# Kernel optimization log

Hardware: AMD Instinct MI355X
Metric: run time of the kernel (lower is better)

Reference implementation:

```python
import jax, jax.numpy as jnp
import numpy as np

N, E, G = 20000, 100000, 32
HID, HEADS, HC = 64, 8, 64  # hidden, heads, per-head channels (PyG: out_channels per head)
L, K = 3, 4


def setup_inputs() -> dict:
    key = jax.random.key(0)
    ks = jax.random.split(key, 20)
    rn = lambda k, s, sc=0.05: jax.random.normal(k, s, jnp.float32) * sc
    HO = HEADS * HC  # 512
    return {
        "x": jax.random.uniform(ks[0], (N, 7), jnp.float32),
        "edge_attr": jax.random.normal(ks[1], (E, 4), jnp.float32),
        "means": jax.random.normal(ks[2], (K, 8), jnp.float32),
        "log_stds": jnp.zeros((K, 8), jnp.float32),
        "sp_W": rn(ks[3], (K, HID), 0.3), "sp_b": jnp.zeros((HID,), jnp.float32),
        "ne_W": rn(ks[4], (7, HID), 0.3), "ne_b": jnp.zeros((HID,), jnp.float32),
        "ee_W": rn(ks[5], (4, HID), 0.3), "ee_b": jnp.zeros((HID,), jnp.float32),
        "Wq": rn(ks[6], (L, HID, HO)), "bq": jnp.zeros((L, HO), jnp.float32),
        "Wk": rn(ks[7], (L, HID, HO)), "bk": jnp.zeros((L, HO), jnp.float32),
        "Wv": rn(ks[8], (L, HID, HO)), "bv": jnp.zeros((L, HO), jnp.float32),
        "We": rn(ks[9], (L, HID, HO)), "be": jnp.zeros((L, HO), jnp.float32),
        "Ws": rn(ks[10], (L, HID, HID)), "bs": jnp.zeros((L, HID), jnp.float32),
        "eu_W": rn(ks[11], (L, 3 * HID, HID)), "eu_b": jnp.zeros((L, HID), jnp.float32),
        "rW1": rn(ks[12], (2 * HID, HID)), "rb1": jnp.zeros((HID,), jnp.float32),
        "rW2": rn(ks[13], (HID, HID)), "rb2": jnp.zeros((HID,), jnp.float32),
        "rW3": rn(ks[14], (HID, 2)), "rb3": jnp.zeros((2,), jnp.float32),
        "edge_index": jax.random.randint(ks[15], (2, E), 0, N, jnp.int32),
        "batch": jnp.sort(jax.random.randint(ks[16], (N,), 0, G, jnp.int32)),
        "num_graphs": G,
    }


def reference(x, edge_attr, means, log_stds, sp_W, sp_b, ne_W, ne_b, ee_W, ee_b,
              Wq, bq, Wk, bk, Wv, bv, We, be, Ws, bs, eu_W, eu_b,
              rW1, rb1, rW2, rb2, rW3, rb3, edge_index, batch, num_graphs):
    n = x.shape[0]
    src, dst = edge_index[0], edge_index[1]

    # ---- SpatialGaussianEncoder (dropout is identity in eval) ----
    p = x[:, :4]
    sl, sr = p[src, :2], p[src, 2:4]
    dl, dr = p[dst, :2], p[dst, 2:4]
    rel = jnp.stack([dl - sl, dl - sr, dr - sl, dr - sr], axis=1)  # [E,4,2]
    dist = jnp.linalg.norm(rel, axis=-1)                           # [E,4]
    ang = jnp.arctan2(rel[..., 1], rel[..., 0])                    # [E,4]
    u = jnp.stack([dist, ang], axis=-1).reshape(-1, 8)             # [E,8] (d,a)x4
    std = jnp.exp(log_stds) + 1e-6                                 # [K,8]
    z = (u[:, None, :] - means[None]) / std[None]                  # [E,K,8]
    w = jnp.exp(-0.5 * jnp.sum(z * z, axis=-1))                    # [E,K]
    sp = jax.nn.relu(w @ sp_W + sp_b)                              # [E,HID]

    h = jax.nn.relu(x @ ne_W + ne_b)                               # [N,HID]
    ea = jax.nn.relu(edge_attr @ ee_W + ee_b) + sp                 # [E,HID]

    scale = 1.0 / float(np.sqrt(HC))
    for l in range(L):
        # PyG TransformerConv(hidden, hidden, heads=8, edge_dim=hidden, concat=False)
        q = (h @ Wq[l] + bq[l]).reshape(n, HEADS, HC)
        k = (h @ Wk[l] + bk[l]).reshape(n, HEADS, HC)
        v = (h @ Wv[l] + bv[l]).reshape(n, HEADS, HC)
        e = (ea @ We[l] + be[l]).reshape(-1, HEADS, HC)
        kj = k[src] + e                                            # [E,H,C]
        alpha = jnp.einsum('ehc,ehc->eh', q[dst], kj) * scale      # [E,H]
        m = jax.ops.segment_max(alpha, dst, num_segments=n)
        ex = jnp.exp(alpha - m[dst])
        den = jax.ops.segment_sum(ex, dst, num_segments=n)
        a = ex / (den[dst] + 1e-16)                                # scatter-softmax over dst
        msg = a[:, :, None] * (v[src] + e)                         # [E,H,C]
        out = jax.ops.segment_sum(msg, dst, num_segments=n).mean(axis=1)  # concat=False -> head mean
        h = jax.nn.relu(out + h @ Ws[l] + bs[l])                   # skip (root_weight) + F.relu
        ef = jnp.concatenate([h[src], h[dst], ea], axis=1)         # [E,3*HID]
        ea = jax.nn.relu(ef @ eu_W[l] + eu_b[l])

    # ---- per-graph masked-mean pooling == segment mean ----
    cn = jnp.maximum(jax.ops.segment_sum(jnp.ones((n,), x.dtype), batch, num_segments=num_graphs), 1.0)
    node_pool = jax.ops.segment_sum(h, batch, num_segments=num_graphs) / cn[:, None]
    eb = batch[src]
    ce = jnp.maximum(jax.ops.segment_sum(jnp.ones((src.shape[0],), x.dtype), eb, num_segments=num_graphs), 1.0)
    edge_pool = jax.ops.segment_sum(ea, eb, num_segments=num_graphs) / ce[:, None]
    g = jnp.concatenate([node_pool, edge_pool], axis=1)            # [G,2*HID]

    h1 = jax.nn.relu(g @ rW1 + rb1)
    h2 = jax.nn.relu(h1 @ rW2 + rb2)
    return jnp.tanh(h2 @ rW3 + rb3)                                # [G,2]
```

## Files before the change

kernel.cpp:

```cpp
#include <hip/hip_runtime.h>
#include <hip/hip_bf16.h>
#include <cstdint>
#include <cstddef>



__global__ void __launch_bounds__(256) k_node_embed(
    const float* __restrict__ x, const float* __restrict__ neW, const float* __restrict__ neb,
    float* __restrict__ h, int N)
{
    int idx = blockIdx.x * 256 + threadIdx.x;
    int n = idx >> 6, c = idx & 63;
    if (n >= N) return;
    float acc = neb[c];
    #pragma unroll
    for (int j = 0; j < 7; ++j) acc += x[(size_t)n * 7 + j] * neW[j * 64 + c];
    h[(size_t)n * 64 + c] = fmaxf(acc, 0.f);
}

__global__ void __launch_bounds__(256) k_edge_w(
    const float* __restrict__ x,
    const float* __restrict__ means, const float* __restrict__ log_stds,
    const int* __restrict__ src, const int* __restrict__ dst,
    float* __restrict__ wbuf, int E)
{
    int e = blockIdx.x * 256 + threadIdx.x;
    if (e >= E) return;
    int s = src[e], d = dst[e];
    const float* ps = x + (size_t)s * 7;
    const float* pd = x + (size_t)d * 7;
    float slx = ps[0], sly = ps[1], srx = ps[2], sry = ps[3];
    float dlx = pd[0], dly = pd[1], drx = pd[2], dry = pd[3];
    float u[8];
    float rx, ry;
    rx = dlx - slx; ry = dly - sly; u[0] = sqrtf(rx*rx + ry*ry); u[1] = atan2f(ry, rx);
    rx = dlx - srx; ry = dly - sry; u[2] = sqrtf(rx*rx + ry*ry); u[3] = atan2f(ry, rx);
    rx = drx - slx; ry = dry - sly; u[4] = sqrtf(rx*rx + ry*ry); u[5] = atan2f(ry, rx);
    rx = drx - srx; ry = dry - sry; u[6] = sqrtf(rx*rx + ry*ry); u[7] = atan2f(ry, rx);
    #pragma unroll
    for (int kk = 0; kk < 4; ++kk) {
        float ssum = 0.f;
        #pragma unroll
        for (int dd = 0; dd < 8; ++dd) {
            float stdv = expf(log_stds[kk*8+dd]) + 1e-6f;
            float z = (u[dd] - means[kk*8+dd]) / stdv;
            ssum += z * z;
        }
        wbuf[(size_t)e*4 + kk] = expf(-0.5f * ssum);
    }
}

__global__ void __launch_bounds__(256) k_edge_ea(
    const float* __restrict__ edge_attr, const float* __restrict__ wbuf,
    const float* __restrict__ spW, const float* __restrict__ spb,
    const float* __restrict__ eeW, const float* __restrict__ eeb,
    float* __restrict__ ea, int E)
{
    int idx = blockIdx.x * 256 + threadIdx.x;
    int e = idx >> 6, c = idx & 63;
    if (e >= E) return;
    float acce = eeb[c];
    #pragma unroll
    for (int j = 0; j < 4; ++j) acce += edge_attr[(size_t)e*4 + j] * eeW[j*64 + c];
    float accs = spb[c];
    #pragma unroll
    for (int j = 0; j < 4; ++j) accs += wbuf[(size_t)e*4 + j] * spW[j*64 + c];
    ea[(size_t)e*64 + c] = fmaxf(acce, 0.f) + fmaxf(accs, 0.f);
}


__global__ void __launch_bounds__(256) k_hist(
    const int* __restrict__ dst, int* __restrict__ deg, int E)
{
    int e = blockIdx.x * 256 + threadIdx.x;
    if (e < E) atomicAdd(deg + dst[e], 1);
}

__global__ void __launch_bounds__(1024) k_scan(
    const int* __restrict__ deg, int* __restrict__ ptr, int* __restrict__ headw, int N)
{
    __shared__ int part[1024];
    int t = threadIdx.x;
    int per = (N + 1023) / 1024;
    int s = 0;
    for (int i = 0; i < per; ++i) { int idx = t*per + i; if (idx < N) s += deg[idx]; }
    part[t] = s;
    __syncthreads();
    for (int off = 1; off < 1024; off <<= 1) {
        int v = (t >= off) ? part[t - off] : 0;
        __syncthreads();
        part[t] += v;
        __syncthreads();
    }
    int base = (t > 0) ? part[t - 1] : 0;
    for (int i = 0; i < per; ++i) {
        int idx = t*per + i;
        if (idx < N) { ptr[idx] = base; headw[idx] = base; base += deg[idx]; }
    }
    if (t == 1023) ptr[N] = part[1023];
}

__global__ void __launch_bounds__(256) k_scatter(
    const int* __restrict__ dst, const int* __restrict__ src, const int* __restrict__ batch,
    int* __restrict__ headw, int* __restrict__ perm, int* __restrict__ srcg,
    int* __restrict__ ieb, int E)
{
    int e = blockIdx.x * 256 + threadIdx.x;
    if (e < E) {
        int s = src[e];
        int pos = atomicAdd(headw + dst[e], 1);
        perm[pos] = e;
        srcg[pos] = s;
        ieb[e] = batch[s];
    }
}


__global__ void __launch_bounds__(256) k_wprod_all(
    const float* __restrict__ Wq, const float* __restrict__ bq,
    const float* __restrict__ Wk, const float* __restrict__ We,
    float* __restrict__ Mk, float* __restrict__ Me,
    float* __restrict__ bqk, float* __restrict__ bqe)
{
    int h = blockIdx.x;
    int which = blockIdx.y;
    int l = blockIdx.z;
    const float* Wq_l = Wq + (size_t)l * 64 * 512;
    const float* bq_l = bq + (size_t)l * 512;
    const float* Wx_l = (which ? We : Wk) + (size_t)l * 64 * 512;
    float* M  = (which ? Me : Mk) + (size_t)l * 64 * 512;
    float* bM = (which ? bqe : bqk) + (size_t)l * 512;
    __shared__ float wq_s[65][64];
    __shared__ float wx_s[64][65];
    int tid = threadIdx.x;
    for (int i = tid; i < 4096; i += 256) {
        int r = i >> 6, c2 = i & 63;
        wq_s[r][c2] = Wq_l[(size_t)r*512 + h*64 + c2];
        wx_s[r][c2] = Wx_l[(size_t)r*512 + h*64 + c2];
    }
    if (tid < 64) wq_s[64][tid] = bq_l[h*64 + tid];
    __syncthreads();
    int j = tid & 63, cg = tid >> 6;
    for (int c = cg*16; c < cg*16 + 16; ++c) {
        float s = 0.f;
        #pragma unroll 8
        for (int c2 = 0; c2 < 64; ++c2) s += wq_s[c][c2] * wx_s[j][c2];
        M[(size_t)c*512 + h*64 + j] = s;
    }
    if (tid < 64) {
        float s = 0.f;
        #pragma unroll 8
        for (int c2 = 0; c2 < 64; ++c2) s += wq_s[64][c2] * wx_s[tid][c2];
        bM[h*64 + tid] = s;
    }
}

__global__ void __launch_bounds__(64) k_wqb_all(
    const float* __restrict__ Wq, const float* __restrict__ bq,
    const float* __restrict__ bk, const float* __restrict__ be,
    float* __restrict__ wqb, float* __restrict__ cb)
{
    int l = blockIdx.x;
    const float* Wq_l = Wq + (size_t)l * 64 * 512;
    const float* bq_l = bq + (size_t)l * 512;
    const float* bk_l = bk + (size_t)l * 512;
    const float* be_l = be + (size_t)l * 512;
    float* wqb_l = wqb + (size_t)l * 512;
    float* cb_l  = cb + (size_t)l * 8;
    int c = threadIdx.x;
    for (int h = 0; h < 8; ++h) {
        float s = 0.f;
        for (int c2 = 0; c2 < 64; ++c2)
            s += Wq_l[(size_t)c*512 + h*64 + c2] * (bk_l[h*64+c2] + be_l[h*64+c2]);
        wqb_l[c*8 + h] = s;
    }
    if (c < 8) {
        float s = 0.f;
        for (int c2 = 0; c2 < 64; ++c2)
            s += bq_l[c*64 + c2] * (bk_l[c*64+c2] + be_l[c*64+c2]);
        cb_l[c] = s;
    }
}

__global__ void __launch_bounds__(256) k_qb(
    const float* __restrict__ h, const float* __restrict__ wqb, const float* __restrict__ cb,
    float* __restrict__ qbv, int N)
{
    int idx = blockIdx.x * 256 + threadIdx.x;
    int n = idx >> 3, hh = idx & 7;
    if (n >= N) return;
    float s = cb[hh];
    #pragma unroll 8
    for (int c = 0; c < 64; ++c) s += h[(size_t)n*64 + c] * wqb[c*8 + hh];
    qbv[(size_t)n*8 + hh] = s;
}


__global__ void __launch_bounds__(256) k_gemm512_dual(
    const float* __restrict__ X,
    const float* __restrict__ W0, const float* __restrict__ b0p, float* __restrict__ Y0,
    const float* __restrict__ W1, const float* __restrict__ b1p, float* __restrict__ Y1,
    int M)
{
    const float* W    = blockIdx.y ? W1 : W0;
    const float* bias = blockIdx.y ? b1p : b0p;
    float* Y          = blockIdx.y ? Y1 : Y0;
    __shared__ __align__(16) float xs[32][64];
    int tid = threadIdx.x;
    int r0 = blockIdx.x * 32;
    for (int i = tid; i < 2048; i += 256) {
        int r = i >> 6, c = i & 63;
        int rr = r0 + r;
        xs[r][c] = (rr < M) ? X[(size_t)rr * 64 + c] : 0.f;
    }
    __syncthreads();
    int wv = tid >> 6, lane = tid & 63;
    int c0 = lane * 8;
    float acc[8][8];
    float4 b0 = *(const float4*)(bias + c0);
    float4 b1 = *(const float4*)(bias + c0 + 4);
    #pragma unroll
    for (int t = 0; t < 8; ++t) {
        acc[t][0]=b0.x; acc[t][1]=b0.y; acc[t][2]=b0.z; acc[t][3]=b0.w;
        acc[t][4]=b1.x; acc[t][5]=b1.y; acc[t][6]=b1.z; acc[t][7]=b1.w;
    }
    #pragma unroll 2
    for (int j = 0; j < 64; ++j) {
        float4 wa = *(const float4*)(W + (size_t)j*512 + c0);
        float4 wb = *(const float4*)(W + (size_t)j*512 + c0 + 4);
        #pragma unroll
        for (int t = 0; t < 8; ++t) {
            float a = xs[wv*8 + t][j];
            acc[t][0] += a*wa.x; acc[t][1] += a*wa.y; acc[t][2] += a*wa.z; acc[t][3] += a*wa.w;
            acc[t][4] += a*wb.x; acc[t][5] += a*wb.y; acc[t][6] += a*wb.z; acc[t][7] += a*wb.w;
        }
    }
    #pragma unroll
    for (int t = 0; t < 8; ++t) {
        int r = r0 + wv*8 + t;
        if (r < M) {
            float4 o0 = {acc[t][0],acc[t][1],acc[t][2],acc[t][3]};
            float4 o1 = {acc[t][4],acc[t][5],acc[t][6],acc[t][7]};
            *(float4*)(Y + (size_t)r*512 + c0)     = o0;
            *(float4*)(Y + (size_t)r*512 + c0 + 4) = o1;
        }
    }
}


__global__ void __launch_bounds__(256) k_attn_fused(
    const float* __restrict__ qk, const float* __restrict__ qe2, const float* __restrict__ qbv,
    const float* __restrict__ ea, const float* __restrict__ hbuf,
    const int* __restrict__ ptr, const int* __restrict__ perm, const int* __restrict__ srcg,
    float* __restrict__ hagg, float* __restrict__ tbuf, float* __restrict__ sbuf, int N)
{
    int wv = threadIdx.x >> 6, lane = threadIdx.x & 63;
    int n = blockIdx.x * 4 + wv;
    if (n >= N) return;
    int h = lane >> 3, p = lane & 7;
    int b = ptr[n], e_ = ptr[n + 1];
    const float4* xp = (const float4*)(qk + (size_t)n*512 + lane*8);
    float4 x0 = xp[0], x1 = xp[1];
    const float4* gp = (const float4*)(qe2 + (size_t)n*512 + lane*8);
    float4 g0 = gp[0], g1 = gp[1];
    float qbh = qbv[(size_t)n*8 + h];
    float m = -3.4e38f, den = 0.f;
    float hacc[8], tacc[8];
    #pragma unroll
    for (int i = 0; i < 8; ++i) { hacc[i] = 0.f; tacc[i] = 0.f; }
    for (int it = b; it < e_; ++it) {
        int s = srcg[it];
        int e = perm[it];
        const float4* hp = (const float4*)(hbuf + (size_t)s*64 + p*8);
        float4 h0 = hp[0], h1 = hp[1];
        const float4* ap = (const float4*)(ea + (size_t)e*64 + p*8);
        float4 a0 = ap[0], a1 = ap[1];
        float t = x0.x*h0.x + x0.y*h0.y + x0.z*h0.z + x0.w*h0.w
                + x1.x*h1.x + x1.y*h1.y + x1.z*h1.z + x1.w*h1.w
                + g0.x*a0.x + g0.y*a0.y + g0.z*a0.z + g0.w*a0.w
                + g1.x*a1.x + g1.y*a1.y + g1.z*a1.z + g1.w*a1.w;
        t += __shfl_xor(t, 1);
        t += __shfl_xor(t, 2);
        t += __shfl_xor(t, 4);
        float al = 0.125f * (t + qbh);
        float mn = fmaxf(m, al);
        float r = expf(m - mn);
        float w = expf(al - mn);
        den = den * r + w;
        m = mn;
        hacc[0] = hacc[0]*r + w*h0.x; hacc[1] = hacc[1]*r + w*h0.y;
        hacc[2] = hacc[2]*r + w*h0.z; hacc[3] = hacc[3]*r + w*h0.w;
        hacc[4] = hacc[4]*r + w*h1.x; hacc[5] = hacc[5]*r + w*h1.y;
        hacc[6] = hacc[6]*r + w*h1.z; hacc[7] = hacc[7]*r + w*h1.w;
        tacc[0] = tacc[0]*r + w*a0.x; tacc[1] = tacc[1]*r + w*a0.y;
        tacc[2] = tacc[2]*r + w*a0.z; tacc[3] = tacc[3]*r + w*a0.w;
        tacc[4] = tacc[4]*r + w*a1.x; tacc[5] = tacc[5]*r + w*a1.y;
        tacc[6] = tacc[6]*r + w*a1.z; tacc[7] = tacc[7]*r + w*a1.w;
    }
    float inv = 0.125f / (den + 1e-16f);
    float4 o;
    o = {hacc[0]*inv,hacc[1]*inv,hacc[2]*inv,hacc[3]*inv};
    *(float4*)(hagg + (size_t)n*512 + lane*8)     = o;
    o = {hacc[4]*inv,hacc[5]*inv,hacc[6]*inv,hacc[7]*inv};
    *(float4*)(hagg + (size_t)n*512 + lane*8 + 4) = o;
    o = {tacc[0]*inv,tacc[1]*inv,tacc[2]*inv,tacc[3]*inv};
    *(float4*)(tbuf + (size_t)n*512 + lane*8)     = o;
    o = {tacc[4]*inv,tacc[5]*inv,tacc[6]*inv,tacc[7]*inv};
    *(float4*)(tbuf + (size_t)n*512 + lane*8 + 4) = o;
    if (p == 0) sbuf[(size_t)n*8 + h] = den * inv;
}

__global__ void __launch_bounds__(256) k_nf_gemm2(
    const float* __restrict__ tbuf, const float* __restrict__ hagg,
    const float* __restrict__ We, const float* __restrict__ Wv,
    float* __restrict__ pbuf, int N)
{
    __shared__ float As[64][132];
    __shared__ __align__(16) float Wt[64][64];
    int tid = threadIdx.x;
    int g = blockIdx.y;
    int n0 = blockIdx.x * 128;
    int wv = tid >> 6, lane = tid & 63;
    int rg = lane >> 3, cg = lane & 7;
    int c0 = cg * 8;
    int rbase = wv * 32 + rg * 4;
    float acc[4][8];
    #pragma unroll
    for (int t = 0; t < 4; ++t)
        #pragma unroll
        for (int i = 0; i < 8; ++i) acc[t][i] = 0.f;
    #pragma unroll
    for (int yy = 0; yy < 2; ++yy) {
        int y = g * 2 + yy;
        #pragma unroll
        for (int round = 0; round < 2; ++round) {
            const float* A = round ? hagg : tbuf;
            const float* W = round ? Wv : We;
            {
                int rt = tid & 127;
                int n = n0 + rt;
                int jh = (tid >> 7) * 32;
                if (n < N) {
                    const float* ap = A + (size_t)n*512 + y*64;
                    #pragma unroll
                    for (int j4 = 0; j4 < 8; ++j4) {
                        int j = jh + j4 * 4;
                        float4 a = *(const float4*)(ap + j);
                        As[j+0][rt] = a.x; As[j+1][rt] = a.y;
                        As[j+2][rt] = a.z; As[j+3][rt] = a.w;
                    }
                } else {
                    #pragma unroll
                    for (int j4 = 0; j4 < 8; ++j4) {
                        int j = jh + j4 * 4;
                        As[j+0][rt] = 0.f; As[j+1][rt] = 0.f;
                        As[j+2][rt] = 0.f; As[j+3][rt] = 0.f;
                    }
                }
                #pragma unroll
                for (int i = 0; i < 4; ++i) {
                    int idx = tid + i * 256;
                    int j = idx >> 4, c4 = (idx & 15) * 4;
                    *(float4*)&Wt[j][c4] = *(const float4*)(W + (size_t)j*512 + y*64 + c4);
                }
            }
            __syncthreads();
            #pragma unroll 4
            for (int j = 0; j < 64; ++j) {
                float4 av = *(const float4*)&As[j][rbase];
                float4 w0 = *(const float4*)&Wt[j][c0];
                float4 w1 = *(const float4*)&Wt[j][c0 + 4];
                acc[0][0] += av.x*w0.x; acc[0][1] += av.x*w0.y; acc[0][2] += av.x*w0.z; acc[0][3] += av.x*w0.w;
                acc[0][4] += av.x*w1.x; acc[0][5] += av.x*w1.y; acc[0][6] += av.x*w1.z; acc[0][7] += av.x*w1.w;
                acc[1][0] += av.y*w0.x; acc[1][1] += av.y*w0.y; acc[1][2] += av.y*w0.z; acc[1][3] += av.y*w0.w;
                acc[1][4] += av.y*w1.x; acc[1][5] += av.y*w1.y; acc[1][6] += av.y*w1.z; acc[1][7] += av.y*w1.w;
                acc[2][0] += av.z*w0.x; acc[2][1] += av.z*w0.y; acc[2][2] += av.z*w0.z; acc[2][3] += av.z*w0.w;
                acc[2][4] += av.z*w1.x; acc[2][5] += av.z*w1.y; acc[2][6] += av.z*w1.z; acc[2][7] += av.z*w1.w;
                acc[3][0] += av.w*w0.x; acc[3][1] += av.w*w0.y; acc[3][2] += av.w*w0.z; acc[3][3] += av.w*w0.w;
                acc[3][4] += av.w*w1.x; acc[3][5] += av.w*w1.y; acc[3][6] += av.w*w1.z; acc[3][7] += av.w*w1.w;
            }
            __syncthreads();
        }
    }
    float* out = pbuf + (size_t)g * N * 64;
    #pragma unroll
    for (int t = 0; t < 4; ++t) {
        int n = n0 + rbase + t;
        if (n < N) {
            float4 o0 = {acc[t][0],acc[t][1],acc[t][2],acc[t][3]};
            float4 o1 = {acc[t][4],acc[t][5],acc[t][6],acc[t][7]};
            *(float4*)(out + (size_t)n*64 + c0)     = o0;
            *(float4*)(out + (size_t)n*64 + c0 + 4) = o1;
        }
    }
}

__global__ void __launch_bounds__(256) k_nf_reduce2(
    const float* __restrict__ pbuf, const float* __restrict__ hin,
    const float* __restrict__ sbuf, const float* __restrict__ Ws,
    const float* __restrict__ be, const float* __restrict__ bv,
    const float* __restrict__ bs, float* __restrict__ hnext, int N)
{
    int idx = blockIdx.x * 256 + threadIdx.x;
    int n = idx >> 6, cc = idx & 63;
    if (n >= N) return;
    float a = bs[cc];
    #pragma unroll
    for (int y = 0; y < 4; ++y) a += pbuf[(size_t)y*N*64 + (size_t)n*64 + cc];
    float hv = hin[(size_t)n*64 + cc];
    #pragma unroll 8
    for (int j = 0; j < 64; ++j) a += __shfl(hv, j) * Ws[(size_t)j*64 + cc];
    #pragma unroll
    for (int h = 0; h < 8; ++h)
        a += sbuf[(size_t)n*8 + h] * (be[h*64 + cc] + bv[h*64 + cc]);
    hnext[(size_t)n*64 + cc] = fmaxf(a, 0.f);
}

__global__ void __launch_bounds__(256) k_eu_pre(
    const float* __restrict__ h, const float* __restrict__ euW,
    float* __restrict__ hw, int N)
{
    __shared__ float As[64][132];
    __shared__ __align__(16) float Wt[64][64];
    int tid = threadIdx.x;
    int y = blockIdx.y;
    int n0 = blockIdx.x * 128;
    {
        int rt = tid & 127;
        int n = n0 + rt;
        int jh = (tid >> 7) * 32;
        if (n < N) {
            const float* ap = h + (size_t)n*64;
            #pragma unroll
            for (int j4 = 0; j4 < 8; ++j4) {
                int j = jh + j4 * 4;
                float4 a = *(const float4*)(ap + j);
                As[j+0][rt] = a.x; As[j+1][rt] = a.y;
                As[j+2][rt] = a.z; As[j+3][rt] = a.w;
            }
        } else {
            #pragma unroll
            for (int j4 = 0; j4 < 8; ++j4) {
                int j = jh + j4 * 4;
                As[j+0][rt] = 0.f; As[j+1][rt] = 0.f;
                As[j+2][rt] = 0.f; As[j+3][rt] = 0.f;
            }
        }
        #pragma unroll
        for (int i = 0; i < 4; ++i) {
            int idx = tid + i * 256;
            *(float4*)&Wt[idx >> 4][(idx & 15) * 4] =
                *(const float4*)(euW + (size_t)y*4096 + idx * 4);
        }
    }
    __syncthreads();
    int wv = tid >> 6, lane = tid & 63;
    int rg = lane >> 3, cg = lane & 7;
    int c0 = cg * 8;
    int rbase = wv * 32 + rg * 4;
    float acc[4][8];
    #pragma unroll
    for (int t = 0; t < 4; ++t)
        #pragma unroll
        for (int i = 0; i < 8; ++i) acc[t][i] = 0.f;
    #pragma unroll 4
    for (int j = 0; j < 64; ++j) {
        float4 av = *(const float4*)&As[j][rbase];
        float4 w0 = *(const float4*)&Wt[j][c0];
        float4 w1 = *(const float4*)&Wt[j][c0 + 4];
        acc[0][0] += av.x*w0.x; acc[0][1] += av.x*w0.y; acc[0][2] += av.x*w0.z; acc[0][3] += av.x*w0.w;
        acc[0][4] += av.x*w1.x; acc[0][5] += av.x*w1.y; acc[0][6] += av.x*w1.z; acc[0][7] += av.x*w1.w;
        acc[1][0] += av.y*w0.x; acc[1][1] += av.y*w0.y; acc[1][2] += av.y*w0.z; acc[1][3] += av.y*w0.w;
        acc[1][4] += av.y*w1.x; acc[1][5] += av.y*w1.y; acc[1][6] += av.y*w1.z; acc[1][7] += av.y*w1.w;
        acc[2][0] += av.z*w0.x; acc[2][1] += av.z*w0.y; acc[2][2] += av.z*w0.z; acc[2][3] += av.z*w0.w;
        acc[2][4] += av.z*w1.x; acc[2][5] += av.z*w1.y; acc[2][6] += av.z*w1.z; acc[2][7] += av.z*w1.w;
        acc[3][0] += av.w*w0.x; acc[3][1] += av.w*w0.y; acc[3][2] += av.w*w0.z; acc[3][3] += av.w*w0.w;
        acc[3][4] += av.w*w1.x; acc[3][5] += av.w*w1.y; acc[3][6] += av.w*w1.z; acc[3][7] += av.w*w1.w;
    }
    #pragma unroll
    for (int t = 0; t < 4; ++t) {
        int n = n0 + rbase + t;
        if (n < N) {
            float4 o0 = {acc[t][0],acc[t][1],acc[t][2],acc[t][3]};
            float4 o1 = {acc[t][4],acc[t][5],acc[t][6],acc[t][7]};
            *(float4*)(hw + (size_t)n*128 + y*64 + c0)     = o0;
            *(float4*)(hw + (size_t)n*128 + y*64 + c0 + 4) = o1;
        }
    }
}

__global__ void __launch_bounds__(256) k_edge_update2(
    const float* __restrict__ hw, const float* __restrict__ ea,
    const float* __restrict__ euW2, const float* __restrict__ eub,
    const int* __restrict__ src, const int* __restrict__ dst,
    float* __restrict__ ea2, int E)
{
    __shared__ float As[64][132];
    __shared__ __align__(16) float Wt[64][64];
    __shared__ int sid[128], did[128];
    int tid = threadIdx.x;
    int e0 = blockIdx.x * 128;
    if (tid < 128) {
        int e = e0 + tid; if (e >= E) e = E - 1;
        sid[tid] = src[e]; did[tid] = dst[e];
    }
    {
        int et = tid & 127;
        int e = e0 + et; if (e >= E) e = E - 1;
        const float* ap = ea + (size_t)e * 64;
        int jh = (tid >> 7) * 32;
        #pragma unroll
        for (int j4 = 0; j4 < 8; ++j4) {
            int j = jh + j4 * 4;
            float4 a = *(const float4*)(ap + j);
            As[j+0][et] = a.x; As[j+1][et] = a.y;
            As[j+2][et] = a.z; As[j+3][et] = a.w;
        }
        #pragma unroll
        for (int i = 0; i < 4; ++i) {
            int idx = tid + i * 256;
            *(float4*)&Wt[idx >> 4][(idx & 15) * 4] = *(const float4*)(euW2 + idx * 4);
        }
    }
    __syncthreads();
    int wv = tid >> 6, lane = tid & 63;
    int rg = lane >> 3, cg = lane & 7;
    int c0 = cg * 8;
    int rbase = wv * 32 + rg * 4;
    float acc[4][8];
    float4 b0 = *(const float4*)(eub + c0);
    float4 b1 = *(const float4*)(eub + c0 + 4);
    #pragma unroll
    for (int t = 0; t < 4; ++t) {
        acc[t][0]=b0.x; acc[t][1]=b0.y; acc[t][2]=b0.z; acc[t][3]=b0.w;
        acc[t][4]=b1.x; acc[t][5]=b1.y; acc[t][6]=b1.z; acc[t][7]=b1.w;
    }
    #pragma unroll 4
    for (int j = 0; j < 64; ++j) {
        float4 av = *(const float4*)&As[j][rbase];
        float4 w0 = *(const float4*)&Wt[j][c0];
        float4 w1 = *(const float4*)&Wt[j][c0 + 4];
        acc[0][0] += av.x*w0.x; acc[0][1] += av.x*w0.y; acc[0][2] += av.x*w0.z; acc[0][3] += av.x*w0.w;
        acc[0][4] += av.x*w1.x; acc[0][5] += av.x*w1.y; acc[0][6] += av.x*w1.z; acc[0][7] += av.x*w1.w;
        acc[1][0] += av.y*w0.x; acc[1][1] += av.y*w0.y; acc[1][2] += av.y*w0.z; acc[1][3] += av.y*w0.w;
        acc[1][4] += av.y*w1.x; acc[1][5] += av.y*w1.y; acc[1][6] += av.y*w1.z; acc[1][7] += av.y*w1.w;
        acc[2][0] += av.z*w0.x; acc[2][1] += av.z*w0.y; acc[2][2] += av.z*w0.z; acc[2][3] += av.z*w0.w;
        acc[2][4] += av.z*w1.x; acc[2][5] += av.z*w1.y; acc[2][6] += av.z*w1.z; acc[2][7] += av.z*w1.w;
        acc[3][0] += av.w*w0.x; acc[3][1] += av.w*w0.y; acc[3][2] += av.w*w0.z; acc[3][3] += av.w*w0.w;
        acc[3][4] += av.w*w1.x; acc[3][5] += av.w*w1.y; acc[3][6] += av.w*w1.z; acc[3][7] += av.w*w1.w;
    }
    #pragma unroll
    for (int t = 0; t < 4; ++t) {
        int e = e0 + rbase + t;
        if (e < E) {
            int s = sid[rbase + t], d = did[rbase + t];
            const float4* sp = (const float4*)(hw + (size_t)s*128 + c0);
            const float4* dp = (const float4*)(hw + (size_t)d*128 + 64 + c0);
            float4 s0 = sp[0], s1 = sp[1];
            float4 d0 = dp[0], d1 = dp[1];
            float4 o0 = {fmaxf(acc[t][0]+s0.x+d0.x,0.f), fmaxf(acc[t][1]+s0.y+d0.y,0.f),
                         fmaxf(acc[t][2]+s0.z+d0.z,0.f), fmaxf(acc[t][3]+s0.w+d0.w,0.f)};
            float4 o1 = {fmaxf(acc[t][4]+s1.x+d1.x,0.f), fmaxf(acc[t][5]+s1.y+d1.y,0.f),
                         fmaxf(acc[t][6]+s1.z+d1.z,0.f), fmaxf(acc[t][7]+s1.w+d1.w,0.f)};
            *(float4*)(ea2 + (size_t)e*64 + c0)     = o0;
            *(float4*)(ea2 + (size_t)e*64 + c0 + 4) = o1;
        }
    }
}


__global__ void __launch_bounds__(64) k_node_pool(
    const float* __restrict__ h, const int* __restrict__ batch,
    float* __restrict__ npool, float* __restrict__ cn, int N)
{
    int lane = threadIdx.x;
    int n0 = blockIdx.x * 64;
    float acc = 0.f; int cur = -1; int run = 0;
    for (int i = 0; i < 64; ++i) {
        int n = n0 + i;
        if (n >= N) break;
        int b = batch[n];
        if (b != cur) {
            if (cur >= 0) {
                atomicAdd(npool + (size_t)cur*64 + lane, acc);
                if (lane == 0) atomicAdd(cn + cur, (float)run);
            }
            cur = b; acc = 0.f; run = 0;
        }
        acc += h[(size_t)n*64 + lane];
        ++run;
    }
    if (cur >= 0) {
        atomicAdd(npool + (size_t)cur*64 + lane, acc);
        if (lane == 0) atomicAdd(cn + cur, (float)run);
    }
}

__global__ void __launch_bounds__(256) k_edge_pool2(
    const float* __restrict__ ea, const int* __restrict__ ieb,
    float* __restrict__ rep, int E)
{
    __shared__ float pool_s[32][64];
    __shared__ float cnt_s[32];
    int tid = threadIdx.x;
    for (int i = tid; i < 2048; i += 256) ((float*)pool_s)[i] = 0.f;
    if (tid < 32) cnt_s[tid] = 0.f;
    __syncthreads();
    int wv = tid >> 6, lane = tid & 63;
    int base = blockIdx.x * 64 + wv * 16;
    int b16[16]; float v16[16];
    #pragma unroll
    for (int u = 0; u < 16; ++u) {
        int e = base + u;
        bool ok = (e < E);
        b16[u] = ok ? ieb[e] : -1;
        v16[u] = ok ? ea[(size_t)e*64 + lane] : 0.f;
    }
    #pragma unroll
    for (int u = 0; u < 16; ++u) {
        if (b16[u] >= 0) {
            atomicAdd(&pool_s[b16[u]][lane], v16[u]);
            if (lane == 0) atomicAdd(&cnt_s[b16[u]], 1.f);
        }
    }
    __syncthreads();
    float* myrep = rep + (size_t)(blockIdx.x & 7) * 2080;
    for (int i = tid; i < 2048; i += 256) atomicAdd(myrep + i, ((float*)pool_s)[i]);
    if (tid < 32) atomicAdd(myrep + 2048 + tid, cnt_s[tid]);
}

__global__ void __launch_bounds__(256) k_pool_merge(
    const float* __restrict__ rep, float* __restrict__ epool, float* __restrict__ ce)
{
    int i = blockIdx.x * 256 + threadIdx.x;
    if (i < 2080) {
        float s = 0.f;
        #pragma unroll
        for (int r = 0; r < 8; ++r) s += rep[(size_t)r*2080 + i];
        if (i < 2048) epool[i] = s; else ce[i - 2048] = s;
    }
}

__global__ void __launch_bounds__(64) k_head_mlp(
    const float* __restrict__ npool, const float* __restrict__ epool,
    const float* __restrict__ cn, const float* __restrict__ ce,
    const float* __restrict__ rW1, const float* __restrict__ rb1,
    const float* __restrict__ rW2, const float* __restrict__ rb2,
    const float* __restrict__ rW3, const float* __restrict__ rb3,
    float* __restrict__ out)
{
    __shared__ float g[128];
    __shared__ float h1[64];
    __shared__ float h2[64];
    int b = blockIdx.x, lane = threadIdx.x;
    float cnv = fmaxf(cn[b], 1.f), cev = fmaxf(ce[b], 1.f);
    g[lane]      = npool[(size_t)b*64 + lane] / cnv;
    g[64 + lane] = epool[(size_t)b*64 + lane] / cev;
    __syncthreads();
    float acc = rb1[lane];
    #pragma unroll 4
    for (int j = 0; j < 128; ++j) acc += g[j] * rW1[j*64 + lane];
    h1[lane] = fmaxf(acc, 0.f);
    __syncthreads();
    acc = rb2[lane];
    #pragma unroll 4
    for (int j = 0; j < 64; ++j) acc += h1[j] * rW2[j*64 + lane];
    h2[lane] = fmaxf(acc, 0.f);
    __syncthreads();
    if (lane < 2) {
        float o = rb3[lane];
        for (int j = 0; j < 64; ++j) o += h2[j] * rW3[j*2 + lane];
        out[b*2 + lane] = tanhf(o);
    }
}


extern "C" void kernel_launch(void* const* d_in, const int* in_sizes, int n_in,
                              void* d_out, int out_size, void* d_ws, size_t ws_size,
                              hipStream_t stream)
{
    const float* x         = (const float*)d_in[0];
    const float* edge_attr = (const float*)d_in[1];
    const float* means     = (const float*)d_in[2];
    const float* log_stds  = (const float*)d_in[3];
    const float* spW       = (const float*)d_in[4];
    const float* spb       = (const float*)d_in[5];
    const float* neW       = (const float*)d_in[6];
    const float* neb       = (const float*)d_in[7];
    const float* eeW       = (const float*)d_in[8];
    const float* eeb       = (const float*)d_in[9];
    const float* Wq        = (const float*)d_in[10];
    const float* bq        = (const float*)d_in[11];
    const float* Wk        = (const float*)d_in[12];
    const float* bk        = (const float*)d_in[13];
    const float* Wv        = (const float*)d_in[14];
    const float* bv        = (const float*)d_in[15];
    const float* We        = (const float*)d_in[16];
    const float* be        = (const float*)d_in[17];
    const float* Ws        = (const float*)d_in[18];
    const float* bs        = (const float*)d_in[19];
    const float* euW       = (const float*)d_in[20];
    const float* eub       = (const float*)d_in[21];
    const float* rW1       = (const float*)d_in[22];
    const float* rb1       = (const float*)d_in[23];
    const float* rW2       = (const float*)d_in[24];
    const float* rb2       = (const float*)d_in[25];
    const float* rW3       = (const float*)d_in[26];
    const float* rb3       = (const float*)d_in[27];
    const int* eidx        = (const int*)d_in[28];
    const int* batch       = (const int*)d_in[29];

    int N = in_sizes[0] / 7;
    int E = in_sizes[1] / 4;
    const int G = 32;
    const int* srcp = eidx;
    const int* dstp = eidx + E;

    float* ws = (float*)d_ws;
    size_t fl = 0;
    float* hA    = ws + fl; fl += (size_t)N * 64;
    float* hB    = ws + fl; fl += (size_t)N * 64;
    float* eaA   = ws + fl; fl += (size_t)E * 64;
    float* eaB   = ws + fl; fl += (size_t)E * 64;
    float* B1    = ws + fl; fl += (size_t)N * 512;
    float* B2    = ws + fl; fl += (size_t)N * 512;
    float* B3    = ws + fl; fl += (size_t)N * 512;
    float* alpha = ws + fl; fl += (size_t)E * 8;
    float* sbuf  = ws + fl; fl += (size_t)N * 8;
    float* qbv   = ws + fl; fl += (size_t)N * 8;
    float* npool = ws + fl; fl += (size_t)G * 64;
    float* epool = ws + fl; fl += (size_t)G * 64;
    float* cn    = ws + fl; fl += G;
    float* ce    = ws + fl; fl += G;
    float* Mk3   = ws + fl; fl += 3 * 64 * 512;
    float* Me3   = ws + fl; fl += 3 * 64 * 512;
    float* bqk3  = ws + fl; fl += 3 * 512;
    float* bqe3  = ws + fl; fl += 3 * 512;
    float* wqb3  = ws + fl; fl += 3 * 512;
    float* cb3   = ws + fl; fl += 24;
    float* rep   = ws + fl; fl += 8 * 2080;
    int* ideg  = (int*)(ws + fl); fl += (size_t)N;
    int* iptr  = (int*)(ws + fl); fl += (size_t)N + 1;
    int* ihead = (int*)(ws + fl); fl += (size_t)N;
    int* iperm = (int*)(ws + fl); fl += (size_t)E;
    int* isrcg = (int*)(ws + fl); fl += (size_t)E;
    int* ieb   = (int*)(ws + fl); fl += (size_t)E;

    float* wbuf = alpha;

    hipMemsetAsync(npool, 0, (size_t)(G * 130) * sizeof(float), stream);
    hipMemsetAsync(rep, 0, (size_t)(8 * 2080) * sizeof(float), stream);
    hipMemsetAsync(ideg, 0, (size_t)N * sizeof(int), stream);

    k_node_embed<<<(N * 64 + 255) / 256, 256, 0, stream>>>(x, neW, neb, hA, N);
    k_edge_w<<<(E + 255) / 256, 256, 0, stream>>>(x, means, log_stds, srcp, dstp, wbuf, E);
    k_edge_ea<<<((size_t)E * 64 + 255) / 256, 256, 0, stream>>>(edge_attr, wbuf,
                                                                spW, spb, eeW, eeb, eaA, E);
    k_hist<<<(E + 255) / 256, 256, 0, stream>>>(dstp, ideg, E);
    k_scan<<<1, 1024, 0, stream>>>(ideg, iptr, ihead, N);
    k_scatter<<<(E + 255) / 256, 256, 0, stream>>>(dstp, srcp, batch, ihead, iperm, isrcg, ieb, E);
    k_wprod_all<<<dim3(8, 2, 3), 256, 0, stream>>>(Wq, bq, Wk, We, Mk3, Me3, bqk3, bqe3);
    k_wqb_all<<<3, 64, 0, stream>>>(Wq, bq, bk, be, wqb3, cb3);

    float* hcur = hA;  float* hnext = hB;
    float* eacur = eaA; float* eanext = eaB;
    for (int l = 0; l < 3; ++l) {
        const float* Wv_l = Wv + (size_t)l * 64 * 512;
        const float* We_l = We + (size_t)l * 64 * 512;
        const float* bv_l = bv + (size_t)l * 512;
        const float* be_l = be + (size_t)l * 512;
        const float* euW_l = euW + (size_t)l * 192 * 64;

        k_gemm512_dual<<<dim3((N + 31) / 32, 2), 256, 0, stream>>>(
            hcur,
            Mk3 + (size_t)l * 32768, bqk3 + (size_t)l * 512, B1,
            Me3 + (size_t)l * 32768, bqe3 + (size_t)l * 512, B2, N);
        k_qb<<<((size_t)N * 8 + 255) / 256, 256, 0, stream>>>(hcur, wqb3 + (size_t)l * 512,
                                                              cb3 + (size_t)l * 8, qbv, N);

        k_attn_fused<<<(N + 3) / 4, 256, 0, stream>>>(B1, B2, qbv, eacur, hcur,
                                                      iptr, iperm, isrcg,
                                                      B1 , B2 , sbuf, N);
        k_nf_gemm2<<<dim3((N + 127) / 128, 4), 256, 0, stream>>>(B2, B1, We_l, Wv_l, B3, N);
        k_nf_reduce2<<<((size_t)N * 64 + 255) / 256, 256, 0, stream>>>(B3, hcur, sbuf,
                                                                       Ws + (size_t)l * 64 * 64,
                                                                       be_l, bv_l,
                                                                       bs + (size_t)l * 64,
                                                                       hnext, N);
        k_eu_pre<<<dim3((N + 127) / 128, 2), 256, 0, stream>>>(hnext, euW_l, B3, N);
        k_edge_update2<<<(E + 127) / 128, 256, 0, stream>>>(B3, eacur, euW_l + 2 * 4096,
                                                            eub + (size_t)l * 64,
                                                            srcp, dstp, eanext, E);
        float* t1 = hcur; hcur = hnext; hnext = t1;
        float* t2 = eacur; eacur = eanext; eanext = t2;
    }

    k_node_pool<<<(N + 63) / 64, 64, 0, stream>>>(hcur, batch, npool, cn, N);
    k_edge_pool2<<<(E + 63) / 64, 256, 0, stream>>>(eacur, ieb, rep, E);
    k_pool_merge<<<9, 256, 0, stream>>>(rep, epool, ce);
    k_head_mlp<<<G, 64, 0, stream>>>(npool, epool, cn, ce, rW1, rb1, rW2, rb2, rW3, rb3,
                                     (float*)d_out);
}
```

Before: 763.0 us.

## Retile 512-wide projection GEMM with shared weight tiles and fuse qb into attention

Replaces the dual 512-column projection GEMM with a kernel that splits output columns into 64-wide slices across a 16-way grid. Each block stages 128 transposed rows of h and a 64x64 weight tile in LDS, so weights are read from shared memory instead of global memory on every iteration. The separate per-node q·b kernel is removed, and its dot product is computed inside the attention kernel with a shuffle reduction, which drops one launch and the qbv buffer round trip. In exchange, h is reloaded once per column slice, and attention does a little extra work per node.

```diff
diff --git a/kernel.cpp b/kernel.cpp
--- a/kernel.cpp
+++ b/kernel.cpp
@@ -182,74 +182,93 @@
     }
 }
 
-__global__ void __launch_bounds__(256) k_qb(
-    const float* __restrict__ h, const float* __restrict__ wqb, const float* __restrict__ cb,
-    float* __restrict__ qbv, int N)
-{
-    int idx = blockIdx.x * 256 + threadIdx.x;
-    int n = idx >> 3, hh = idx & 7;
-    if (n >= N) return;
-    float s = cb[hh];
-    #pragma unroll 8
-    for (int c = 0; c < 64; ++c) s += h[(size_t)n*64 + c] * wqb[c*8 + hh];
-    qbv[(size_t)n*8 + hh] = s;
-}
-
-
-__global__ void __launch_bounds__(256) k_gemm512_dual(
-    const float* __restrict__ X,
-    const float* __restrict__ W0, const float* __restrict__ b0p, float* __restrict__ Y0,
-    const float* __restrict__ W1, const float* __restrict__ b1p, float* __restrict__ Y1,
-    int M)
-{
-    const float* W    = blockIdx.y ? W1 : W0;
-    const float* bias = blockIdx.y ? b1p : b0p;
-    float* Y          = blockIdx.y ? Y1 : Y0;
-    __shared__ __align__(16) float xs[32][64];
+
+__global__ void __launch_bounds__(256) k_proj16(
+    const float* __restrict__ h,
+    const float* __restrict__ Mk, const float* __restrict__ bqk, float* __restrict__ qk,
+    const float* __restrict__ Me, const float* __restrict__ bqe, float* __restrict__ qe2,
+    int N)
+{
+    __shared__ float As[64][132];
+    __shared__ __align__(16) float Wt[64][64];
     int tid = threadIdx.x;
-    int r0 = blockIdx.x * 32;
-    for (int i = tid; i < 2048; i += 256) {
-        int r = i >> 6, c = i & 63;
-        int rr = r0 + r;
-        xs[r][c] = (rr < M) ? X[(size_t)rr * 64 + c] : 0.f;
+    int y = blockIdx.y;
+    int which = y >> 3, yb = y & 7;
+    const float* W    = which ? Me : Mk;
+    const float* bias = (which ? bqe : bqk) + yb * 64;
+    float* Y          = which ? qe2 : qk;
+    int n0 = blockIdx.x * 128;
+    {
+        int rt = tid & 127;
+        int n = n0 + rt;
+        int jh = (tid >> 7) * 32;
+        if (n < N) {
+            const float* ap = h + (size_t)n*64;
+            #pragma unroll
+            for (int j4 = 0; j4 < 8; ++j4) {
+                int j = jh + j4 * 4;
+                float4 a = *(const float4*)(ap + j);
+                As[j+0][rt] = a.x; As[j+1][rt] = a.y;
+                As[j+2][rt] = a.z; As[j+3][rt] = a.w;
+            }
+        } else {
+            #pragma unroll
+            for (int j4 = 0; j4 < 8; ++j4) {
+                int j = jh + j4 * 4;
+                As[j+0][rt] = 0.f; As[j+1][rt] = 0.f;
+                As[j+2][rt] = 0.f; As[j+3][rt] = 0.f;
+            }
+        }
+        #pragma unroll
+        for (int i = 0; i < 4; ++i) {
+            int idx = tid + i * 256;
+            int j = idx >> 4, c4 = (idx & 15) * 4;
+            *(float4*)&Wt[j][c4] = *(const float4*)(W + (size_t)j*512 + yb*64 + c4);
+        }
     }
     __syncthreads();
     int wv = tid >> 6, lane = tid & 63;
-    int c0 = lane * 8;
-    float acc[8][8];
+    int rg = lane >> 3, cg = lane & 7;
+    int c0 = cg * 8;
+    int rbase = wv * 32 + rg * 4;
+    float acc[4][8];
     float4 b0 = *(const float4*)(bias + c0);
     float4 b1 = *(const float4*)(bias + c0 + 4);
     #pragma unroll
-    for (int t = 0; t < 8; ++t) {
+    for (int t = 0; t < 4; ++t) {
         acc[t][0]=b0.x; acc[t][1]=b0.y; acc[t][2]=b0.z; acc[t][3]=b0.w;
         acc[t][4]=b1.x; acc[t][5]=b1.y; acc[t][6]=b1.z; acc[t][7]=b1.w;
     }
-    #pragma unroll 2
+    #pragma unroll 4
     for (int j = 0; j < 64; ++j) {
-        float4 wa = *(const float4*)(W + (size_t)j*512 + c0);
-        float4 wb = *(const float4*)(W + (size_t)j*512 + c0 + 4);
-        #pragma unroll
-        for (int t = 0; t < 8; ++t) {
-            float a = xs[wv*8 + t][j];
-            acc[t][0] += a*wa.x; acc[t][1] += a*wa.y; acc[t][2] += a*wa.z; acc[t][3] += a*wa.w;
-            acc[t][4] += a*wb.x; acc[t][5] += a*wb.y; acc[t][6] += a*wb.z; acc[t][7] += a*wb.w;
-        }
-    }
-    #pragma unroll
-    for (int t = 0; t < 8; ++t) {
-        int r = r0 + wv*8 + t;
-        if (r < M) {
+        float4 av = *(const float4*)&As[j][rbase];
+        float4 w0 = *(const float4*)&Wt[j][c0];
+        float4 w1 = *(const float4*)&Wt[j][c0 + 4];
+        acc[0][0] += av.x*w0.x; acc[0][1] += av.x*w0.y; acc[0][2] += av.x*w0.z; acc[0][3] += av.x*w0.w;
+        acc[0][4] += av.x*w1.x; acc[0][5] += av.x*w1.y; acc[0][6] += av.x*w1.z; acc[0][7] += av.x*w1.w;
+        acc[1][0] += av.y*w0.x; acc[1][1] += av.y*w0.y; acc[1][2] += av.y*w0.z; acc[1][3] += av.y*w0.w;
+        acc[1][4] += av.y*w1.x; acc[1][5] += av.y*w1.y; acc[1][6] += av.y*w1.z; acc[1][7] += av.y*w1.w;
+        acc[2][0] += av.z*w0.x; acc[2][1] += av.z*w0.y; acc[2][2] += av.z*w0.z; acc[2][3] += av.z*w0.w;
+        acc[2][4] += av.z*w1.x; acc[2][5] += av.z*w1.y; acc[2][6] += av.z*w1.z; acc[2][7] += av.z*w1.w;
+        acc[3][0] += av.w*w0.x; acc[3][1] += av.w*w0.y; acc[3][2] += av.w*w0.z; acc[3][3] += av.w*w0.w;
+        acc[3][4] += av.w*w1.x; acc[3][5] += av.w*w1.y; acc[3][6] += av.w*w1.z; acc[3][7] += av.w*w1.w;
+    }
+    #pragma unroll
+    for (int t = 0; t < 4; ++t) {
+        int n = n0 + rbase + t;
+        if (n < N) {
             float4 o0 = {acc[t][0],acc[t][1],acc[t][2],acc[t][3]};
             float4 o1 = {acc[t][4],acc[t][5],acc[t][6],acc[t][7]};
-            *(float4*)(Y + (size_t)r*512 + c0)     = o0;
-            *(float4*)(Y + (size_t)r*512 + c0 + 4) = o1;
+            *(float4*)(Y + (size_t)n*512 + yb*64 + c0)     = o0;
+            *(float4*)(Y + (size_t)n*512 + yb*64 + c0 + 4) = o1;
         }
     }
 }
 
 
 __global__ void __launch_bounds__(256) k_attn_fused(
-    const float* __restrict__ qk, const float* __restrict__ qe2, const float* __restrict__ qbv,
+    const float* __restrict__ qk, const float* __restrict__ qe2,
+    const float* __restrict__ wqb, const float* __restrict__ cb,
     const float* __restrict__ ea, const float* __restrict__ hbuf,
     const int* __restrict__ ptr, const int* __restrict__ perm, const int* __restrict__ srcg,
     float* __restrict__ hagg, float* __restrict__ tbuf, float* __restrict__ sbuf, int N)
@@ -263,7 +282,16 @@
     float4 x0 = xp[0], x1 = xp[1];
     const float4* gp = (const float4*)(qe2 + (size_t)n*512 + lane*8);
     float4 g0 = gp[0], g1 = gp[1];
-    float qbh = qbv[(size_t)n*8 + h];
+    const float4* hdp = (const float4*)(hbuf + (size_t)n*64 + p*8);
+    float4 hd0 = hdp[0], hd1 = hdp[1];
+    float qbh = hd0.x*wqb[(p*8+0)*8+h] + hd0.y*wqb[(p*8+1)*8+h]
+              + hd0.z*wqb[(p*8+2)*8+h] + hd0.w*wqb[(p*8+3)*8+h]
+              + hd1.x*wqb[(p*8+4)*8+h] + hd1.y*wqb[(p*8+5)*8+h]
+              + hd1.z*wqb[(p*8+6)*8+h] + hd1.w*wqb[(p*8+7)*8+h];
+    qbh += __shfl_xor(qbh, 1);
+    qbh += __shfl_xor(qbh, 2);
+    qbh += __shfl_xor(qbh, 4);
+    qbh += cb[h];
     float m = -3.4e38f, den = 0.f;
     float hacc[8], tacc[8];
     #pragma unroll
@@ -727,7 +755,6 @@
     float* B3    = ws + fl; fl += (size_t)N * 512;
     float* alpha = ws + fl; fl += (size_t)E * 8;
     float* sbuf  = ws + fl; fl += (size_t)N * 8;
-    float* qbv   = ws + fl; fl += (size_t)N * 8;
     float* npool = ws + fl; fl += (size_t)G * 64;
     float* epool = ws + fl; fl += (size_t)G * 64;
     float* cn    = ws + fl; fl += G;
@@ -771,14 +798,15 @@
         const float* be_l = be + (size_t)l * 512;
         const float* euW_l = euW + (size_t)l * 192 * 64;
 
-        k_gemm512_dual<<<dim3((N + 31) / 32, 2), 256, 0, stream>>>(
+        k_proj16<<<dim3((N + 127) / 128, 16), 256, 0, stream>>>(
             hcur,
             Mk3 + (size_t)l * 32768, bqk3 + (size_t)l * 512, B1,
             Me3 + (size_t)l * 32768, bqe3 + (size_t)l * 512, B2, N);
-        k_qb<<<((size_t)N * 8 + 255) / 256, 256, 0, stream>>>(hcur, wqb3 + (size_t)l * 512,
-                                                              cb3 + (size_t)l * 8, qbv, N);
-
-        k_attn_fused<<<(N + 3) / 4, 256, 0, stream>>>(B1, B2, qbv, eacur, hcur,
+
+        k_attn_fused<<<(N + 3) / 4, 256, 0, stream>>>(B1, B2,
+                                                      wqb3 + (size_t)l * 512,
+                                                      cb3 + (size_t)l * 8,
+                                                      eacur, hcur,
                                                       iptr, iperm, isrcg,
                                                       B1 , B2 , sbuf, N);
         k_nf_gemm2<<<dim3((N + 127) / 128, 4), 256, 0, stream>>>(B2, B1, We_l, Wv_l, B3, N);
```

Result: no change. 750.0 us (-1.7%).
